# Kernel optimization log

Hardware: AMD Instinct MI355X
Metric: run time of the kernel (lower is better)

## Reference

```python
import jax, jax.numpy as jnp
import numpy as np

M = 4096       # number of graphs (rows of h)
N = 262144     # total nodes across the batch
DH = 128       # d_h
DX = 128       # d_x

def setup_inputs() -> dict:
    key = jax.random.key(0)
    k1, k2, k3, k4 = jax.random.split(key, 4)
    h = jax.random.normal(k1, (M, DH), dtype=jnp.float32)
    x = jax.random.normal(k2, (N, DX), dtype=jnp.float32)
    a = 0.001 * jax.random.uniform(k3, (DH, DX), dtype=jnp.float32)  # nn.Parameter init
    segment_ids = jnp.sort(jax.random.randint(k4, (N,), 0, M))  # ragged graph membership
    return {"h": h, "x": x, "a": a, "segment_ids": segment_ids}

def reference(h, x, a, segment_ids):
    # proj[g] = h[g] @ a, broadcast to nodes via segment_ids (== repeat_interleave by batch_num_nodes)
    proj = h @ a                                    # (m, d_x)
    s = jnp.sum(x * proj[segment_ids], axis=1)      # (n,) per-node score
    # segment softmax (max for stability, exp, sum)
    smax = jax.ops.segment_max(s, segment_ids, num_segments=M)
    smax = jnp.where(jnp.isfinite(smax), smax, 0.0)  # guard empty segments
    e = jnp.exp(s - smax[segment_ids])              # (n,)
    z = jax.ops.segment_sum(e, segment_ids, num_segments=M)
    att = e / z[segment_ids]                        # (n,) normalized attention
    # weighted sum of node features per graph
    return jax.ops.segment_sum(att[:, None] * x, segment_ids, num_segments=M)  # (m, d_x)
```

## Files before the change

### kernel.cpp

```cpp
#include <hip/hip_runtime.h>
#include <math.h>

#define MSEG  4096
#define NNODE 262144
#define DDIM  128
#define CH    16
#define SEG_PER_BLK 4
#define PROJ_ROWS 16

__global__ __launch_bounds__(256) void seg_starts_kernel(
    const int* __restrict__ seg, int* __restrict__ starts)
{
    int i = blockIdx.x * blockDim.x + threadIdx.x;
    if (i >= NNODE) return;
    int s = seg[i];
    int prev = (i == 0) ? -1 : seg[i - 1];
    for (int g = prev + 1; g <= s; ++g) starts[g] = i;
    if (i == NNODE - 1)
        for (int g = s + 1; g <= MSEG; ++g) starts[g] = NNODE;
}

__global__ __launch_bounds__(256) void proj_kernel(
    const float* __restrict__ h, const float* __restrict__ a,
    float* __restrict__ proj)
{
    __shared__ __align__(16) float a_lds[DDIM * DDIM];
    __shared__ __align__(16) float h_lds[PROJ_ROWS * DDIM];
    const int tid = threadIdx.x;
    const int g0  = blockIdx.x * PROJ_ROWS;

    const float4* a4  = (const float4*)a;
    float4*       al4 = (float4*)a_lds;
    #pragma unroll
    for (int j = 0; j < (DDIM * DDIM / 4) / 256; ++j)
        al4[j * 256 + tid] = a4[j * 256 + tid];
    const float4* h4  = (const float4*)(h + (size_t)g0 * DDIM);
    float4*       hl4 = (float4*)h_lds;
    #pragma unroll
    for (int j = 0; j < (PROJ_ROWS * DDIM / 4) / 256; ++j)
        hl4[j * 256 + tid] = h4[j * 256 + tid];
    __syncthreads();

    const int dp = tid & 63;
    const int rh = tid >> 6;
    const float2* al2 = (const float2*)a_lds;
    #pragma unroll
    for (int rr = 0; rr < PROJ_ROWS / 4; ++rr) {
        const int r = rh * (PROJ_ROWS / 4) + rr;
        float2 p = make_float2(0.f, 0.f);
        #pragma unroll 8
        for (int k = 0; k < DDIM; ++k) {
            const float  hv = h_lds[r * DDIM + k];
            const float2 av = al2[k * 64 + dp];
            p.x += hv * av.x;
            p.y += hv * av.y;
        }
        ((float2*)(proj + (size_t)(g0 + r) * DDIM))[dp] = p;
    }
}

__global__ __launch_bounds__(256) void attn_seg_kernel(
    const float* __restrict__ x,
    const float* __restrict__ proj,
    const int*   __restrict__ starts,
    float*       __restrict__ out)
{
    const int tid = threadIdx.x;
    const int g   = blockIdx.x * SEG_PER_BLK + (tid >> 6);
    const int L   = tid & 63;
    const int l   = L & 15;
    const int r   = L >> 4;

    const int start = starts[g];
    const int end   = starts[g + 1];
    float4* out4 = (float4*)out;

    if (start >= end) {
        if (r == 0) {
            out4[(size_t)g * 32 + 2 * l]     = make_float4(0.f, 0.f, 0.f, 0.f);
            out4[(size_t)g * 32 + 2 * l + 1] = make_float4(0.f, 0.f, 0.f, 0.f);
        }
        return;
    }

    const float4* __restrict__ x4p = (const float4*)x;
    const float4 pj0 = ((const float4*)proj)[(size_t)g * 32 + 2 * l];
    const float4 pj1 = ((const float4*)proj)[(size_t)g * 32 + 2 * l + 1];

    float m_run = -INFINITY;
    float l_run = 0.f;
    float4 acc0 = make_float4(0.f, 0.f, 0.f, 0.f);
    float4 acc1 = make_float4(0.f, 0.f, 0.f, 0.f);

    int cs  = start;
    int n_c = min(CH, end - cs);
    float4 xv0[4], xv1[4];
    #pragma unroll
    for (int p = 0; p < 4; ++p) {
        const int i = p * 4 + r;
        xv0[p] = make_float4(0.f, 0.f, 0.f, 0.f);
        xv1[p] = make_float4(0.f, 0.f, 0.f, 0.f);
        if (i < n_c) {
            const size_t base = (size_t)(cs + i) * 32 + 2 * l;
            xv0[p] = x4p[base];
            xv1[p] = x4p[base + 1];
        }
    }

    while (true) {
        float sc[4];
        #pragma unroll
        for (int p = 0; p < 4; ++p) {
            float ps = xv0[p].x * pj0.x + xv0[p].y * pj0.y
                     + xv0[p].z * pj0.z + xv0[p].w * pj0.w
                     + xv1[p].x * pj1.x + xv1[p].y * pj1.y
                     + xv1[p].z * pj1.z + xv1[p].w * pj1.w;
            ps += __shfl_xor(ps, 1);
            ps += __shfl_xor(ps, 2);
            ps += __shfl_xor(ps, 4);
            ps += __shfl_xor(ps, 8);
            sc[p] = (p * 4 + r < n_c) ? ps : -INFINITY;
        }
        float mc = fmaxf(fmaxf(sc[0], sc[1]), fmaxf(sc[2], sc[3]));
        mc = fmaxf(mc, __shfl_xor(mc, 16));
        mc = fmaxf(mc, __shfl_xor(mc, 32));
        if (mc - m_run > 30.f) {
            const float alpha = __expf(m_run - mc);
            l_run *= alpha;
            acc0.x *= alpha; acc0.y *= alpha; acc0.z *= alpha; acc0.w *= alpha;
            acc1.x *= alpha; acc1.y *= alpha; acc1.z *= alpha; acc1.w *= alpha;
            m_run = mc;
        }
        float lsum = 0.f;
        #pragma unroll
        for (int p = 0; p < 4; ++p) {
            const bool valid = (p * 4 + r < n_c);
            const float e = valid ? __expf(sc[p] - m_run) : 0.f;
            lsum += e;
            acc0.x += e * xv0[p].x; acc0.y += e * xv0[p].y;
            acc0.z += e * xv0[p].z; acc0.w += e * xv0[p].w;
            acc1.x += e * xv1[p].x; acc1.y += e * xv1[p].y;
            acc1.z += e * xv1[p].z; acc1.w += e * xv1[p].w;
        }
        lsum += __shfl_xor(lsum, 16);
        lsum += __shfl_xor(lsum, 32);
        l_run += lsum;

        cs += CH;
        if (cs >= end) break;
        n_c = min(CH, end - cs);
        #pragma unroll
        for (int p = 0; p < 4; ++p) {
            const int i = p * 4 + r;
            xv0[p] = make_float4(0.f, 0.f, 0.f, 0.f);
            xv1[p] = make_float4(0.f, 0.f, 0.f, 0.f);
            if (i < n_c) {
                const size_t base = (size_t)(cs + i) * 32 + 2 * l;
                xv0[p] = x4p[base];
                xv1[p] = x4p[base + 1];
            }
        }
    }

    acc0.x += __shfl_xor(acc0.x, 16); acc0.y += __shfl_xor(acc0.y, 16);
    acc0.z += __shfl_xor(acc0.z, 16); acc0.w += __shfl_xor(acc0.w, 16);
    acc1.x += __shfl_xor(acc1.x, 16); acc1.y += __shfl_xor(acc1.y, 16);
    acc1.z += __shfl_xor(acc1.z, 16); acc1.w += __shfl_xor(acc1.w, 16);
    acc0.x += __shfl_xor(acc0.x, 32); acc0.y += __shfl_xor(acc0.y, 32);
    acc0.z += __shfl_xor(acc0.z, 32); acc0.w += __shfl_xor(acc0.w, 32);
    acc1.x += __shfl_xor(acc1.x, 32); acc1.y += __shfl_xor(acc1.y, 32);
    acc1.z += __shfl_xor(acc1.z, 32); acc1.w += __shfl_xor(acc1.w, 32);

    if (r == 0) {
        const float inv = 1.f / l_run;
        out4[(size_t)g * 32 + 2 * l] =
            make_float4(acc0.x * inv, acc0.y * inv, acc0.z * inv, acc0.w * inv);
        out4[(size_t)g * 32 + 2 * l + 1] =
            make_float4(acc1.x * inv, acc1.y * inv, acc1.z * inv, acc1.w * inv);
    }
}

extern "C" void kernel_launch(void* const* d_in, const int* in_sizes, int n_in,
                              void* d_out, int out_size, void* d_ws, size_t ws_size,
                              hipStream_t stream) {
    const float* h   = (const float*)d_in[0];
    const float* x   = (const float*)d_in[1];
    const float* a   = (const float*)d_in[2];
    const int*   seg = (const int*)  d_in[3];
    float* out = (float*)d_out;

    int*   starts = (int*)d_ws;
    float* proj   = (float*)((char*)d_ws + 32768);

    seg_starts_kernel<<<(NNODE + 255) / 256, 256, 0, stream>>>(seg, starts);
    proj_kernel<<<MSEG / PROJ_ROWS, 256, 0, stream>>>(h, a, proj);
    attn_seg_kernel<<<MSEG / SEG_PER_BLK, 256, 0, stream>>>(x, proj, starts, out);
}
```

Before: 212.7 us.

## Merge prep kernels, register-block projection rows, coalesce x float4 loads

Folds the segment-start and projection kernels into one launch, with block ranges picking the role, to drop a kernel launch and its serialization. The projection loop now keeps four row accumulators so each LDS read of `a` is reused four times. In the attention kernel each lane now loads float4 indices l and l+16 instead of 2l and 2l+1, so each half-wave reads one contiguous 256-byte span. The seg-start blocks now also reserve the 72KB LDS used by the projection blocks, which may limit how many of them run at once.

```diff
diff --git a/kernel.cpp b/kernel.cpp
--- a/kernel.cpp
+++ b/kernel.cpp
@@ -7,28 +7,30 @@
 #define CH    16
 #define SEG_PER_BLK 4
 #define PROJ_ROWS 16
-
-__global__ __launch_bounds__(256) void seg_starts_kernel(
+#define PROJ_BLOCKS (MSEG / PROJ_ROWS)
+#define SEG_BLOCKS  ((NNODE + 255) / 256)
+
+__global__ __launch_bounds__(256) void prep_kernel(
+    const float* __restrict__ h, const float* __restrict__ a,
+    float* __restrict__ proj,
     const int* __restrict__ seg, int* __restrict__ starts)
-{
-    int i = blockIdx.x * blockDim.x + threadIdx.x;
-    if (i >= NNODE) return;
-    int s = seg[i];
-    int prev = (i == 0) ? -1 : seg[i - 1];
-    for (int g = prev + 1; g <= s; ++g) starts[g] = i;
-    if (i == NNODE - 1)
-        for (int g = s + 1; g <= MSEG; ++g) starts[g] = NNODE;
-}
-
-__global__ __launch_bounds__(256) void proj_kernel(
-    const float* __restrict__ h, const float* __restrict__ a,
-    float* __restrict__ proj)
 {
     __shared__ __align__(16) float a_lds[DDIM * DDIM];
     __shared__ __align__(16) float h_lds[PROJ_ROWS * DDIM];
     const int tid = threadIdx.x;
-    const int g0  = blockIdx.x * PROJ_ROWS;
-
+
+    if (blockIdx.x >= PROJ_BLOCKS) {
+        const int i = (blockIdx.x - PROJ_BLOCKS) * 256 + tid;
+        if (i >= NNODE) return;
+        const int s = seg[i];
+        const int prev = (i == 0) ? -1 : seg[i - 1];
+        for (int g = prev + 1; g <= s; ++g) starts[g] = i;
+        if (i == NNODE - 1)
+            for (int g = s + 1; g <= MSEG; ++g) starts[g] = NNODE;
+        return;
+    }
+
+    const int g0 = blockIdx.x * PROJ_ROWS;
     const float4* a4  = (const float4*)a;
     float4*       al4 = (float4*)a_lds;
     #pragma unroll
@@ -44,19 +46,24 @@
     const int dp = tid & 63;
     const int rh = tid >> 6;
     const float2* al2 = (const float2*)a_lds;
-    #pragma unroll
-    for (int rr = 0; rr < PROJ_ROWS / 4; ++rr) {
-        const int r = rh * (PROJ_ROWS / 4) + rr;
-        float2 p = make_float2(0.f, 0.f);
-        #pragma unroll 8
-        for (int k = 0; k < DDIM; ++k) {
-            const float  hv = h_lds[r * DDIM + k];
-            const float2 av = al2[k * 64 + dp];
-            p.x += hv * av.x;
-            p.y += hv * av.y;
-        }
-        ((float2*)(proj + (size_t)(g0 + r) * DDIM))[dp] = p;
-    }
+    float2 p0 = make_float2(0.f, 0.f), p1 = make_float2(0.f, 0.f);
+    float2 p2 = make_float2(0.f, 0.f), p3 = make_float2(0.f, 0.f);
+    #pragma unroll 8
+    for (int k = 0; k < DDIM; ++k) {
+        const float2 av = al2[k * 64 + dp];
+        const float h0 = h_lds[(rh * 4 + 0) * DDIM + k];
+        const float h1 = h_lds[(rh * 4 + 1) * DDIM + k];
+        const float h2 = h_lds[(rh * 4 + 2) * DDIM + k];
+        const float h3 = h_lds[(rh * 4 + 3) * DDIM + k];
+        p0.x += h0 * av.x; p0.y += h0 * av.y;
+        p1.x += h1 * av.x; p1.y += h1 * av.y;
+        p2.x += h2 * av.x; p2.y += h2 * av.y;
+        p3.x += h3 * av.x; p3.y += h3 * av.y;
+    }
+    ((float2*)(proj + (size_t)(g0 + rh * 4 + 0) * DDIM))[dp] = p0;
+    ((float2*)(proj + (size_t)(g0 + rh * 4 + 1) * DDIM))[dp] = p1;
+    ((float2*)(proj + (size_t)(g0 + rh * 4 + 2) * DDIM))[dp] = p2;
+    ((float2*)(proj + (size_t)(g0 + rh * 4 + 3) * DDIM))[dp] = p3;
 }
 
 __global__ __launch_bounds__(256) void attn_seg_kernel(
@@ -77,15 +84,15 @@
 
     if (start >= end) {
         if (r == 0) {
-            out4[(size_t)g * 32 + 2 * l]     = make_float4(0.f, 0.f, 0.f, 0.f);
-            out4[(size_t)g * 32 + 2 * l + 1] = make_float4(0.f, 0.f, 0.f, 0.f);
+            out4[(size_t)g * 32 + l]      = make_float4(0.f, 0.f, 0.f, 0.f);
+            out4[(size_t)g * 32 + 16 + l] = make_float4(0.f, 0.f, 0.f, 0.f);
         }
         return;
     }
 
     const float4* __restrict__ x4p = (const float4*)x;
-    const float4 pj0 = ((const float4*)proj)[(size_t)g * 32 + 2 * l];
-    const float4 pj1 = ((const float4*)proj)[(size_t)g * 32 + 2 * l + 1];
+    const float4 pj0 = ((const float4*)proj)[(size_t)g * 32 + l];
+    const float4 pj1 = ((const float4*)proj)[(size_t)g * 32 + 16 + l];
 
     float m_run = -INFINITY;
     float l_run = 0.f;
@@ -101,9 +108,9 @@
         xv0[p] = make_float4(0.f, 0.f, 0.f, 0.f);
         xv1[p] = make_float4(0.f, 0.f, 0.f, 0.f);
         if (i < n_c) {
-            const size_t base = (size_t)(cs + i) * 32 + 2 * l;
+            const size_t base = (size_t)(cs + i) * 32 + l;
             xv0[p] = x4p[base];
-            xv1[p] = x4p[base + 1];
+            xv1[p] = x4p[base + 16];
         }
     }
 
@@ -155,9 +162,9 @@
             xv0[p] = make_float4(0.f, 0.f, 0.f, 0.f);
             xv1[p] = make_float4(0.f, 0.f, 0.f, 0.f);
             if (i < n_c) {
-                const size_t base = (size_t)(cs + i) * 32 + 2 * l;
+                const size_t base = (size_t)(cs + i) * 32 + l;
                 xv0[p] = x4p[base];
-                xv1[p] = x4p[base + 1];
+                xv1[p] = x4p[base + 16];
             }
         }
     }
@@ -173,9 +180,9 @@
 
     if (r == 0) {
         const float inv = 1.f / l_run;
-        out4[(size_t)g * 32 + 2 * l] =
+        out4[(size_t)g * 32 + l] =
             make_float4(acc0.x * inv, acc0.y * inv, acc0.z * inv, acc0.w * inv);
-        out4[(size_t)g * 32 + 2 * l + 1] =
+        out4[(size_t)g * 32 + 16 + l] =
             make_float4(acc1.x * inv, acc1.y * inv, acc1.z * inv, acc1.w * inv);
     }
 }
@@ -192,7 +199,6 @@
     int*   starts = (int*)d_ws;
     float* proj   = (float*)((char*)d_ws + 32768);
 
-    seg_starts_kernel<<<(NNODE + 255) / 256, 256, 0, stream>>>(seg, starts);
-    proj_kernel<<<MSEG / PROJ_ROWS, 256, 0, stream>>>(h, a, proj);
+    prep_kernel<<<PROJ_BLOCKS + SEG_BLOCKS, 256, 0, stream>>>(h, a, proj, seg, starts);
     attn_seg_kernel<<<MSEG / SEG_PER_BLK, 256, 0, stream>>>(x, proj, starts, out);
 }
```

Result: faster. 207.7 us (-2.3%).
